# Kernel tuning notes

Hardware: AMD Instinct MI355X
Metric: run time of the kernel (lower is better)

## Reference

```python
import jax, jax.numpy as jnp
import numpy as np

EPS = 1e-08
GUMBEL_TEMP = 1.0
TOPK = 5


def setup_inputs() -> dict:
    key = jax.random.key(0)
    k1, k2, k3, k4, k5, k6 = jax.random.split(key, 6)
    return {
        "h": jax.random.normal(k1, (64, 16), dtype=jnp.float32),
        "input": jax.random.normal(k2, (64, 16), dtype=jnp.float32),
        "w_p": jax.random.normal(k3, (16, 16), dtype=jnp.float32),
        "bias": jax.random.normal(k4, (64, 16), dtype=jnp.float32),
        "U1": jax.random.uniform(k5, (64, 4, 4), dtype=jnp.float32),
        "U2": jax.random.uniform(k6, (64, 4, 4), dtype=jnp.float32),
    }


def reference(h, input, w_p, bias, U1, U2):
    B = input.shape[0]  # 64 (hardcoded in the original module)
    h = h.reshape(B, 16)

    # Conditional range-remap when |h| exceeds 100 (data-dependent -> jnp.where)
    h_min, h_max = jnp.min(h), jnp.max(h)
    out_of_range = (h_max > 100.0) | (h_min < -100.0)
    mapped = jnp.clip((h - h_min) / (h_max - h_min) * 0.6 - 0.3, -0.3, 0.3)
    h = jnp.where(out_of_range, mapped, h)

    # small matmul + bias -> logits, reshaped to (64, 4, 4)
    mask = (h @ w_p + bias).reshape(64, 4, 4)

    # Gumbel noise difference
    g1 = -jnp.log(-jnp.log(U1 + EPS) + EPS)
    g2 = -jnp.log(-jnp.log(U2 + EPS) + EPS)
    soft = jax.nn.sigmoid((mask + g1 - g2) / GUMBEL_TEMP)

    # batched per-row top-k (k=5) over the flattened 4x4 grid
    flat = soft.reshape(64, 16)
    topv, _ = jax.lax.top_k(flat, TOPK)
    fifth = topv[:, TOPK - 1].reshape(64, 1, 1)

    # straight-through hard mask
    hard_bin = (soft >= fifth).astype(soft.dtype)
    hard = jax.lax.stop_gradient(hard_bin - soft) + soft
    return hard
```

## Files before the change

kernel.cpp:

```cpp
#include <hip/hip_runtime.h>
#include <math.h>

#define G_EPS 1e-8f

__global__ __launch_bounds__(1024) void GumbelLinear_kernel(
    const float* __restrict__ h_in,
    const float* __restrict__ w_p,
    const float* __restrict__ bias,
    const float* __restrict__ U1,
    const float* __restrict__ U2,
    float* __restrict__ out)
{
    __shared__ float h_s[64][16];
    __shared__ float w_s[16][16];
    __shared__ float s_s[64][16];
    __shared__ float wmin_s[16];
    __shared__ float wmax_s[16];
    __shared__ float gmm[2];

    const int tid = threadIdx.x;
    const int b   = tid >> 4;
    const int j   = tid & 15;

    float hv = h_in[tid];
    if (tid < 256) w_s[tid >> 4][tid & 15] = w_p[tid];

    float mn = hv, mx = hv;
    #pragma unroll
    for (int off = 32; off > 0; off >>= 1) {
        mn = fminf(mn, __shfl_down(mn, off));
        mx = fmaxf(mx, __shfl_down(mx, off));
    }
    const int lane = tid & 63;
    const int wid  = tid >> 6;
    if (lane == 0) { wmin_s[wid] = mn; wmax_s[wid] = mx; }
    __syncthreads();
    if (tid == 0) {
        float m0 = wmin_s[0], m1 = wmax_s[0];
        #pragma unroll
        for (int i = 1; i < 16; ++i) {
            m0 = fminf(m0, wmin_s[i]);
            m1 = fmaxf(m1, wmax_s[i]);
        }
        gmm[0] = m0; gmm[1] = m1;
    }
    __syncthreads();
    const float gmin = gmm[0], gmax = gmm[1];

    if (gmax > 100.0f || gmin < -100.0f) {
        float m = (hv - gmin) / (gmax - gmin) * 0.6f - 0.3f;
        hv = fminf(fmaxf(m, -0.3f), 0.3f);
    }
    h_s[b][j] = hv;
    __syncthreads();

    float acc = bias[tid];
    #pragma unroll
    for (int k = 0; k < 16; ++k) acc += h_s[b][k] * w_s[k][j];

    const float u1 = U1[tid], u2 = U2[tid];
    const float g1 = -logf(-logf(u1 + G_EPS) + G_EPS);
    const float g2 = -logf(-logf(u2 + G_EPS) + G_EPS);
    const float x  = acc + g1 - g2;
    const float soft = 1.0f / (1.0f + expf(-x));

    s_s[b][j] = soft;
    __syncthreads();

    int cnt = 0;
    #pragma unroll
    for (int k = 0; k < 16; ++k) cnt += (s_s[b][k] > soft) ? 1 : 0;

    const float hb = (cnt <= 4) ? 1.0f : 0.0f;
    out[tid] = (hb - soft) + soft;
}

extern "C" void kernel_launch(void* const* d_in, const int* in_sizes, int n_in,
                              void* d_out, int out_size, void* d_ws, size_t ws_size,
                              hipStream_t stream) {
    const float* h    = (const float*)d_in[0];
    const float* w_p  = (const float*)d_in[2];
    const float* bias = (const float*)d_in[3];
    const float* U1   = (const float*)d_in[4];
    const float* U2   = (const float*)d_in[5];
    float* out = (float*)d_out;

    GumbelLinear_kernel<<<1, 1024, 0, stream>>>(h, w_p, bias, U1, U2, out);
}
```

Baseline: 9.676 us.

## Replace shared-memory staging with wave shuffles and drop sigmoid in top-k

Moves all global loads to the top, loads the weight matrix with float4, and replaces two barriers plus shared h/soft arrays with xor-shuffles inside 16-lane groups for both the matvec and the top-k count. Every thread now does the final min/max reduction itself, which removes one barrier. The ranking runs on pre-sigmoid logits with fast __logf, and the output is written directly as 0/1, dropping the straight-through arithmetic. This can change results where ties or near-ties differ under fast-math logs or sigmoid saturation.

```diff
diff --git a/kernel.cpp b/kernel.cpp
--- a/kernel.cpp
+++ b/kernel.cpp
@@ -11,68 +11,59 @@
     const float* __restrict__ U2,
     float* __restrict__ out)
 {
-    __shared__ float h_s[64][16];
     __shared__ float w_s[16][16];
-    __shared__ float s_s[64][16];
-    __shared__ float wmin_s[16];
-    __shared__ float wmax_s[16];
-    __shared__ float gmm[2];
+    __shared__ float pmin[16], pmax[16];
 
     const int tid = threadIdx.x;
-    const int b   = tid >> 4;
     const int j   = tid & 15;
+    const int wid = tid >> 6;
 
-    float hv = h_in[tid];
-    if (tid < 256) w_s[tid >> 4][tid & 15] = w_p[tid];
+    const float hv = h_in[tid];
+    const float bv = bias[tid];
+    const float u1 = U1[tid];
+    const float u2 = U2[tid];
+    if (tid < 64) {
+        reinterpret_cast<float4*>(&w_s[0][0])[tid] =
+            reinterpret_cast<const float4*>(w_p)[tid];
+    }
 
     float mn = hv, mx = hv;
     #pragma unroll
-    for (int off = 32; off > 0; off >>= 1) {
-        mn = fminf(mn, __shfl_down(mn, off));
-        mx = fmaxf(mx, __shfl_down(mx, off));
+    for (int off = 1; off < 64; off <<= 1) {
+        mn = fminf(mn, __shfl_xor(mn, off));
+        mx = fmaxf(mx, __shfl_xor(mx, off));
     }
-    const int lane = tid & 63;
-    const int wid  = tid >> 6;
-    if (lane == 0) { wmin_s[wid] = mn; wmax_s[wid] = mx; }
+    if ((tid & 63) == 0) { pmin[wid] = mn; pmax[wid] = mx; }
     __syncthreads();
-    if (tid == 0) {
-        float m0 = wmin_s[0], m1 = wmax_s[0];
-        #pragma unroll
-        for (int i = 1; i < 16; ++i) {
-            m0 = fminf(m0, wmin_s[i]);
-            m1 = fmaxf(m1, wmax_s[i]);
-        }
-        gmm[0] = m0; gmm[1] = m1;
+    float gmin = pmin[0], gmax = pmax[0];
+    #pragma unroll
+    for (int i = 1; i < 16; ++i) {
+        gmin = fminf(gmin, pmin[i]);
+        gmax = fmaxf(gmax, pmax[i]);
     }
-    __syncthreads();
-    const float gmin = gmm[0], gmax = gmm[1];
 
+    float hh = hv;
     if (gmax > 100.0f || gmin < -100.0f) {
-        float m = (hv - gmin) / (gmax - gmin) * 0.6f - 0.3f;
-        hv = fminf(fmaxf(m, -0.3f), 0.3f);
+        hh = fminf(fmaxf((hv - gmin) / (gmax - gmin) * 0.6f - 0.3f, -0.3f), 0.3f);
     }
-    h_s[b][j] = hv;
-    __syncthreads();
 
-    float acc = bias[tid];
+    float acc = bv + hh * w_s[j][j];
     #pragma unroll
-    for (int k = 0; k < 16; ++k) acc += h_s[b][k] * w_s[k][j];
+    for (int m = 1; m < 16; ++m) {
+        const float hk = __shfl_xor(hh, m);
+        acc += hk * w_s[j ^ m][j];
+    }
 
-    const float u1 = U1[tid], u2 = U2[tid];
-    const float g1 = -logf(-logf(u1 + G_EPS) + G_EPS);
-    const float g2 = -logf(-logf(u2 + G_EPS) + G_EPS);
-    const float x  = acc + g1 - g2;
-    const float soft = 1.0f / (1.0f + expf(-x));
-
-    s_s[b][j] = soft;
-    __syncthreads();
+    const float x = acc + __logf(-__logf(u2 + G_EPS) + G_EPS)
+                        - __logf(-__logf(u1 + G_EPS) + G_EPS);
 
     int cnt = 0;
     #pragma unroll
-    for (int k = 0; k < 16; ++k) cnt += (s_s[b][k] > soft) ? 1 : 0;
+    for (int m = 1; m < 16; ++m) {
+        cnt += (__shfl_xor(x, m) > x) ? 1 : 0;
+    }
 
-    const float hb = (cnt <= 4) ? 1.0f : 0.0f;
-    out[tid] = (hb - soft) + soft;
+    out[tid] = (cnt <= 4) ? 1.0f : 0.0f;
 }
 
 extern "C" void kernel_launch(void* const* d_in, const int* in_sizes, int n_in,
```

Measured after the change: 9.601 us. About the same (-0.8%).
